# Optimization experiments

Measured on AMD Instinct MI355X. Metric: run time of the kernel, lower is better.

## Reference

```python
import jax, jax.numpy as jnp
import numpy as np

D_IN, HID, HEADS, MAXN, OUT, B = 16, 128, 4, 8, 128, 32768
HD = HID // HEADS
EPS = 1e-5


def _ln(x, g, b):
    m = jnp.mean(x, -1, keepdims=True)
    v = jnp.mean((x - m) ** 2, -1, keepdims=True)
    return (x - m) * jax.lax.rsqrt(v + EPS) * g + b


def _encode(x, enc_w1, enc_b1, enc_g1, enc_be1, enc_w2, enc_b2, enc_g2, enc_be2):
    h = _ln(x @ enc_w1.T + enc_b1, enc_g1, enc_be1)
    h = jax.nn.relu(h)
    return _ln(h @ enc_w2.T + enc_b2, enc_g2, enc_be2)


def setup_inputs() -> dict:
    key = jax.random.key(0)
    ks = jax.random.split(key, 12)

    def xavier(k, shape):
        # xavier_uniform with gain=0.5, matching _init_weights
        lim = 0.5 * np.sqrt(6.0 / (shape[0] + shape[1]))
        return jax.random.uniform(k, shape, jnp.float32, -lim, lim)

    z = lambda n: jnp.zeros((n,), jnp.float32)
    o = lambda n: jnp.ones((n,), jnp.float32)
    return {
        "current_node": jax.random.normal(ks[0], (B, D_IN), jnp.float32),
        "neighbor_nodes": jax.random.normal(ks[1], (B, MAXN, D_IN), jnp.float32),
        "neighbor_mask": jax.random.randint(ks[2], (B, MAXN), 0, 2, jnp.int32),
        "enc_w1": xavier(ks[3], (HID, D_IN)), "enc_b1": z(HID),
        "enc_g1": o(HID), "enc_be1": z(HID),
        "enc_w2": xavier(ks[4], (HID, HID)), "enc_b2": z(HID),
        "enc_g2": o(HID), "enc_be2": z(HID),
        "in_proj_w": xavier(ks[5], (3 * HID, HID)), "in_proj_b": z(3 * HID),
        "out_w": xavier(ks[6], (HID, HID)), "out_b": z(HID),
        "an_g": o(HID), "an_b": z(HID),
        "p1_w": xavier(ks[7], (HID, 2 * HID)), "p1_b": z(HID),
        "p1_g": o(HID), "p1_be": z(HID),
        "p2_w": xavier(ks[8], (OUT, HID)), "p2_b": z(OUT),
        "p2_g": o(OUT), "p2_be": z(OUT),
    }


def _forward(current_node, neighbor_nodes, neighbor_mask,
             enc_w1, enc_b1, enc_g1, enc_be1, enc_w2, enc_b2, enc_g2, enc_be2,
             in_proj_w, in_proj_b, out_w, out_b, an_g, an_b,
             p1_w, p1_b, p1_g, p1_be, p2_w, p2_b, p2_g, p2_be):
    bsz = current_node.shape[0]
    cur_emb = _encode(current_node, enc_w1, enc_b1, enc_g1, enc_be1,
                      enc_w2, enc_b2, enc_g2, enc_be2)                  # [B, HID]
    nb_emb = _encode(neighbor_nodes, enc_w1, enc_b1, enc_g1, enc_be1,
                     enc_w2, enc_b2, enc_g2, enc_be2)                   # [B, N, HID]

    valid = neighbor_mask > 0                                            # [B, N]
    has_nb = jnp.any(valid, axis=1)                                      # [B]

    # MultiheadAttention (eval mode, dropout inactive): q from current node, k/v from neighbors
    wq, wk, wv = in_proj_w[:HID], in_proj_w[HID:2 * HID], in_proj_w[2 * HID:]
    bq, bk, bv = in_proj_b[:HID], in_proj_b[HID:2 * HID], in_proj_b[2 * HID:]
    q = (cur_emb @ wq.T + bq).reshape(bsz, HEADS, HD)                    # [B, H, hd]
    k = (nb_emb @ wk.T + bk).reshape(bsz, MAXN, HEADS, HD)               # [B, N, H, hd]
    v = (nb_emb @ wv.T + bv).reshape(bsz, MAXN, HEADS, HD)

    scores = jnp.einsum('bhd,bnhd->bhn', q, k) / np.sqrt(HD)             # [B, H, N]
    # rows with zero valid neighbors get a fully-open mask to avoid NaN softmax;
    # their attention result is discarded below (replaced by cur_emb)
    safe = jnp.where(has_nb[:, None], valid, True)                       # [B, N]
    scores = jnp.where(safe[:, None, :], scores, -1e9)
    attn = jax.nn.softmax(scores, axis=-1)                               # [B, H, N]
    ctx = jnp.einsum('bhn,bnhd->bhd', attn, v).reshape(bsz, HID)
    ctx = ctx @ out_w.T + out_b
    agg = jnp.where(has_nb[:, None], _ln(ctx, an_g, an_b), cur_emb)      # [B, HID]

    combined = jnp.concatenate([cur_emb, agg], axis=-1)                  # [B, 2*HID]
    h = _ln(combined @ p1_w.T + p1_b, p1_g, p1_be)
    h = jax.nn.relu(h)
    return _ln(h @ p2_w.T + p2_b, p2_g, p2_be)                           # [B, OUT]


def reference(current_node, neighbor_nodes, neighbor_mask,
              enc_w1, enc_b1, enc_g1, enc_be1, enc_w2, enc_b2, enc_g2, enc_be2,
              in_proj_w, in_proj_b, out_w, out_b, an_g, an_b,
              p1_w, p1_b, p1_g, p1_be, p2_w, p2_b, p2_g, p2_be):
    return _forward(current_node, neighbor_nodes, neighbor_mask,
                    enc_w1, enc_b1, enc_g1, enc_be1, enc_w2, enc_b2, enc_g2, enc_be2,
                    in_proj_w, in_proj_b, out_w, out_b, an_g, an_b,
                    p1_w, p1_b, p1_g, p1_be, p2_w, p2_b, p2_g, p2_be)
```

## Files before the change

kernel.cpp:

```cpp
#include <hip/hip_runtime.h>

#define DEV __device__ __forceinline__

typedef __attribute__((ext_vector_type(8))) short bf16x8;
typedef __attribute__((ext_vector_type(4))) float f32x4;

static constexpr int NTH = 512;
static constexpr int TBE = 16;

static constexpr int W1P = 0;
static constexpr int W2  = 4096;
static constexpr int WQ  = 20480;
static constexpr int WK  = 36864;
static constexpr int WVW = 53248;
static constexpr int OW  = 69632;
static constexpr int P1A = 86016;
static constexpr int P1B = 102400;
static constexpr int P2W = 118784;
static constexpr int WS_BF16_TOT = 135168;
static constexpr int NPRM = 18 * 128;
static constexpr int WQr  = 139776;
static constexpr int OWr  = 156160;
static constexpr int P1Ar = 172544;
static constexpr int P1Br = 188928;
// ... 59 lines not shown
    int row = i >> 5, col = i & 31;
    float v = (col < 16) ? enc_w1[row * 16 + col] : 0.f;
    wsb[W1P + row * 32 + ((((col >> 3) ^ (row & 3)) << 3) | (col & 7))] = f2bf(v);
  }
  if (rm) {
    for (int i = t; i < 6 * 16384; i += NT) {
      int mi = i >> 14, e = i & 16383, row = e >> 7, col = e & 127;
      float v; int dstb;
      switch (mi) {
        case 0: v = in_pw[row * 128 + col];         dstb = WQr;  break;
        case 1: v = out_w[row * 128 + col];         dstb = OWr;  break;
        case 2: v = p1_w[row * 256 + col];          dstb = P1Ar; break;
        case 3: v = p1_w[row * 256 + 128 + col];    dstb = P1Br; break;
        case 4: v = p2_w[row * 128 + col];          dstb = P2r;  break;
        default: v = in_pw[(128 + col) * 128 + row]; dstb = WKt; break;
      }
      wsb[dstb + e] = f2bf(v);
    }
  }
  for (int i = t; i < NPRM; i += NT) {
    int s = i >> 7, c = i & 127; float v;
    switch (s) {
      case 0: v = enc_b1[c]; break;  case 1: v = enc_g1[c]; break;
      case 2: v = enc_be1[c]; break; case 3: v = enc_b2[c]; break;
      case 4: v = enc_g2[c]; break;  case 5: v = enc_be2[c]; break;
      case 6: v = in_pb[c]; break;   case 7: v = in_pb[128 + c]; break;
      case 8: v = in_pb[256 + c]; break; case 9: v = out_b[c]; break;
      case 10: v = an_g[c]; break;   case 11: v = an_b[c]; break;
      case 12: v = p1_b[c]; break;   case 13: v = p1_g[c]; break;
      case 14: v = p1_be[c]; break;  case 15: v = p2_b[c]; break;
      case 16: v = p2_g[c]; break;   default: v = p2_be[c]; break;
    }
    wsp[i] = v;
  }
}

__global__ __launch_bounds__(512, 4)
void k1_enc(const float* __restrict__ cur_x, const float* __restrict__ nb_x,
            const unsigned short* __restrict__ wsb, const float* __restrict__ wsp,
            unsigned short* __restrict__ wse) {
  __shared__ __align__(16) unsigned short s_w1[4096];
  __shared__ __align__(16) unsigned short s_w2[16384];
  __shared__ __align__(16) unsigned short s_h1[8][16 * 136];
  __shared__ float s_prm[6 * 128];

  const int tid = threadIdx.x;
  const int wv = tid >> 6, l = tid & 63, l15 = l & 15, lg = l >> 4;

  ((uint4*)s_w1)[tid] = ((const uint4*)(wsb + W1P))[tid];
#pragma unroll
  for (int i = 0; i < 4; ++i)
    ((uint4*)s_w2)[tid + i * 512] = ((const uint4*)(wsb + W2))[tid + i * 512];
  for (int i = tid; i < 768; i += 512) s_prm[i] = wsp[i];
  __syncthreads();

  unsigned short* h1 = &s_h1[wv][0];

  auto ln_t = [&](float (&acc)[8][4], int bs, int gs, int es, bool relu) {
#pragma unroll
    for (int ct = 0; ct < 8; ++ct) {
      float4 bb = *(const float4*)&s_prm[bs * 128 + ct * 16 + lg * 4];
      acc[ct][0] += bb.x; acc[ct][1] += bb.y; acc[ct][2] += bb.z; acc[ct][3] += bb.w;
    }
    float sm = 0.f, sq = 0.f;
#pragma unroll
    for (int ct = 0; ct < 8; ++ct)
#pragma unroll
      for (int r = 0; r < 4; ++r) { sm += acc[ct][r]; sq = fmaf(acc[ct][r], acc[ct][r], sq); }
    sm += __shfl_xor(sm, 16); sq += __shfl_xor(sq, 16);
    sm += __shfl_xor(sm, 32); sq += __shfl_xor(sq, 32);
    float mean = sm * 0.0078125f;
    float var = fmaf(sq, 0.0078125f, -mean * mean);
    float inv = rsqrtf(var + 1e-5f);
#pragma unroll
    for (int ct = 0; ct < 8; ++ct) {
      float4 gg = *(const float4*)&s_prm[gs * 128 + ct * 16 + lg * 4];
      float4 ee = *(const float4*)&s_prm[es * 128 + ct * 16 + lg * 4];
      float ga[4] = {gg.x, gg.y, gg.z, gg.w}, ea[4] = {ee.x, ee.y, ee.z, ee.w};
#pragma unroll
      for (int r = 0; r < 4; ++r) {
        float v = (acc[ct][r] - mean) * inv * ga[r] + ea[r];
        acc[ct][r] = relu ? fmaxf(v, 0.f) : v;
      }
    }
  };

#pragma unroll 1
  for (int t = blockIdx.x * 8 + wv; t < 18432; t += 9216) {
    asm volatile("s_waitcnt lgkmcnt(0)" ::: "memory");
    const bool isnb = t < 16384;
    const float* src = isnb ? nb_x + (size_t)t * 256
                            : cur_x + ((size_t)t - 16384) * 256;
    unsigned short* dst = wse + (isnb ? (size_t)NBE + (size_t)t * 2048
                                      : (size_t)CURE + ((size_t)t - 16384) * 2048);

    float4 fin = ((const float4*)src)[l];
    {
      uint2 u;
      u.x = (unsigned)f2bf(fin.x) | ((unsigned)f2bf(fin.y) << 16);
      u.y = (unsigned)f2bf(fin.z) | ((unsigned)f2bf(fin.w) << 16);
      *(uint2*)(h1 + (l >> 2) * 16 + (l & 3) * 4) = u;
    }
    bf16x8 bx = (bf16x8){0, 0, 0, 0, 0, 0, 0, 0};
    if (lg < 2) bx = *(const bf16x8*)(h1 + l15 * 16 + lg * 8);

    float acc[8][4];
#pragma unroll
    for (int ct = 0; ct < 8; ++ct) {
      f32x4 a = {0.f, 0.f, 0.f, 0.f};
      a = mfma16(frag32(s_w1, ct * 16 + l15, lg), bx, a);
      acc[ct][0] = a[0]; acc[ct][1] = a[1]; acc[ct][2] = a[2]; acc[ct][3] = a[3];
    }
    ln_t(acc, 0, 1, 2, true);
#pragma unroll
    for (int ct = 0; ct < 8; ++ct) {
      uint2 u;
      u.x = (unsigned)f2bf(acc[ct][0]) | ((unsigned)f2bf(acc[ct][1]) << 16);
      u.y = (unsigned)f2bf(acc[ct][2]) | ((unsigned)f2bf(acc[ct][3]) << 16);
      *(uint2*)(h1 + l15 * 136 + ct * 16 + lg * 4) = u;
    }

    bf16x8 bh[4];
#pragma unroll
    for (int kk = 0; kk < 4; ++kk)
      bh[kk] = *(const bf16x8*)(h1 + l15 * 136 + kk * 32 + lg * 8);
#pragma unroll
    for (int ct = 0; ct < 8; ++ct) {
      f32x4 a = {0.f, 0.f, 0.f, 0.f};
#pragma unroll
      for (int kk = 0; kk < 4; ++kk)
        a = mfma16(frag128(s_w2, ct * 16 + l15, kk, lg), bh[kk], a);
      acc[ct][0] = a[0]; acc[ct][1] = a[1]; acc[ct][2] = a[2]; acc[ct][3] = a[3];
    }
    ln_t(acc, 3, 4, 5, false);

#pragma unroll
    for (int ct = 0; ct < 8; ++ct) {
      uint2 u;
      u.x = (unsigned)f2bf(acc[ct][0]) | ((unsigned)f2bf(acc[ct][1]) << 16);
      u.y = (unsigned)f2bf(acc[ct][2]) | ((unsigned)f2bf(acc[ct][3]) << 16);
      int c = ct * 2 + (lg >> 1);
      *(uint2*)(h1 + l15 * 128 + ((c ^ l15) << 3) + (lg & 1) * 4) = u;
    }
#pragma unroll
    for (int i = 0; i < 4; ++i) {
      int R = i * 4 + lg;
      int j = l15;
      uint4 u = *(const uint4*)(h1 + R * 128 + ((j ^ R) << 3));
      ((uint4*)dst)[i * 64 + l] = u;
    }
  }
}

__global__ __launch_bounds__(256, 3)
void k2_head(const int* __restrict__ nb_mask,
             const unsigned short* __restrict__ wsb, const float* __restrict__ wsp,
             float* __restrict__ out) {
  __shared__ __align__(16) unsigned short s_buf[4][2][16 * 136];
  __shared__ float s_prm[NPRM];
  __shared__ int s_mask[64];

  const int tid = threadIdx.x;
  const int wv = tid >> 6, l = tid & 63, l15 = l & 15, lg = l >> 4;
  const int ew = (blockIdx.x * 4 + wv) * 16;
  unsigned short* bufA = &s_buf[wv][0][0];
  unsigned short* bufB = &s_buf[wv][1][0];

  for (int i = tid; i < NPRM; i += 256) s_prm[i] = wsp[i];
  {
    const uint4* src = (const uint4*)(wsb + CURE + (size_t)ew * 128);
#pragma unroll
    for (int i = 0; i < 4; ++i) {
      int idx = i * 64 + l, row = idx >> 4, ch = idx & 15;
      *(uint4*)(bufA + row * 136 + ch * 8) = src[idx];
    }
  }
  if (l < 16) {
    int m = 0; const int* mp = nb_mask + (size_t)(ew + l) * 8;
#pragma unroll
    for (int n = 0; n < 8; ++n) m |= (mp[n] > 0) << n;
    s_mask[wv * 16 + l] = m;
  }
  __syncthreads();

  float acc[8][4];

  auto ln_t = [&](int bs, int gs, int es, bool relu) {
#pragma unroll
    for (int ct = 0; ct < 8; ++ct) {
      float4 bb = *(const float4*)&s_prm[bs * 128 + ct * 16 + lg * 4];
      acc[ct][0] += bb.x; acc[ct][1] += bb.y; acc[ct][2] += bb.z; acc[ct][3] += bb.w;
    }
    float sm = 0.f, sq = 0.f;
#pragma unroll
    for (int ct = 0; ct < 8; ++ct)
#pragma unroll
      for (int r = 0; r < 4; ++r) { sm += acc[ct][r]; sq = fmaf(acc[ct][r], acc[ct][r], sq); }
    sm += __shfl_xor(sm, 16); sq += __shfl_xor(sq, 16);
    sm += __shfl_xor(sm, 32); sq += __shfl_xor(sq, 32);
    float mean = sm * 0.0078125f;
    float var = fmaf(sq, 0.0078125f, -mean * mean);
    float inv = rsqrtf(var + 1e-5f);
#pragma unroll
    for (int ct = 0; ct < 8; ++ct) {
      float4 gg = *(const float4*)&s_prm[gs * 128 + ct * 16 + lg * 4];
      float4 ee = *(const float4*)&s_prm[es * 128 + ct * 16 + lg * 4];
      float ga[4] = {gg.x, gg.y, gg.z, gg.w}, ea[4] = {ee.x, ee.y, ee.z, ee.w};
#pragma unroll
      for (int r = 0; r < 4; ++r) {
        float v = (acc[ct][r] - mean) * inv * ga[r] + ea[r];
        acc[ct][r] = relu ? fmaxf(v, 0.f) : v;
      }
    }
  };

  {
    bf16x8 b[4];
#pragma unroll
    for (int kk = 0; kk < 4; ++kk) b[kk] = *(const bf16x8*)(bufA + l15 * 136 + kk * 32 + lg * 8);
#pragma unroll
    for (int ct = 0; ct < 8; ++ct) {
      f32x4 a4 = {0.f, 0.f, 0.f, 0.f};
#pragma unroll
      for (int kk = 0; kk < 4; ++kk) {
        bf16x8 w = *(const bf16x8*)(wsb + WQr + (ct * 16 + l15) * 128 + kk * 32 + lg * 8);
        a4 = mfma16(w, b[kk], a4);
      }
      float4 bb = *(const float4*)&s_prm[6 * 128 + ct * 16 + lg * 4];
      uint2 u;
      u.x = (unsigned)f2bf((a4[0] + bb.x) * 0.17677669529663687f)
          | ((unsigned)f2bf((a4[1] + bb.y) * 0.17677669529663687f) << 16);
      u.y = (unsigned)f2bf((a4[2] + bb.z) * 0.17677669529663687f)
          | ((unsigned)f2bf((a4[3] + bb.w) * 0.17677669529663687f) << 16);
      *(uint2*)(bufB + l15 * 136 + ct * 16 + lg * 4) = u;
    }
  }
  __builtin_amdgcn_sched_barrier(0);

  bf16x8 qb[4];
#pragma unroll
  for (int h = 0; h < 4; ++h)
    qb[h] = *(const bf16x8*)(bufB + l15 * 136 + h * 32 + lg * 8);
  __builtin_amdgcn_sched_barrier(0);

  bf16x8 qf[4][4];
#pragma unroll
  for (int h = 0; h < 4; ++h) {
#pragma unroll
    for (int ct = 0; ct < 8; ++ct) {
      bf16x8 w = *(const bf16x8*)(wsb + WKt + (ct * 16 + l15) * 128 + h * 32 + lg * 8);
      f32x4 a4 = {0.f, 0.f, 0.f, 0.f};
      a4 = mfma16(w, qb[h], a4);
      uint2 u;
      u.x = (unsigned)f2bf(a4[0]) | ((unsigned)f2bf(a4[1]) << 16);
      u.y = (unsigned)f2bf(a4[2]) | ((unsigned)f2bf(a4[3]) << 16);
      *(uint2*)(bufB + l15 * 136 + ct * 16 + lg * 4) = u;
    }
    __builtin_amdgcn_sched_barrier(0);
#pragma unroll
    for (int kk = 0; kk < 4; ++kk)
      qf[h][kk] = *(const bf16x8*)(bufB + l15 * 136 + kk * 32 + lg * 8);
    __builtin_amdgcn_sched_barrier(0);
  }

  float pe[4][8];
  {
    const unsigned short* nbp = wsb + NBE + (size_t)(ew + l15) * 1024;
    float ps[4][8];
#pragma unroll
    for (int h = 0; h < 4; ++h)
#pragma unroll
      for (int n = 0; n < 8; ++n) ps[h][n] = 0.f;
#pragma unroll
    for (int n = 0; n < 8; ++n) {
#pragma unroll
      for (int kk = 0; kk < 4; ++kk) {
        bf16x8 nf = *(const bf16x8*)(nbp + n * 128 + kk * 32 + lg * 8);
#pragma unroll
        for (int i = 0; i < 8; ++i) {
          float nv = bf2f((unsigned short)nf[i]);
          ps[0][n] = fmaf(nv, bf2f((unsigned short)qf[0][kk][i]), ps[0][n]);
          ps[1][n] = fmaf(nv, bf2f((unsigned short)qf[1][kk][i]), ps[1][n]);
          ps[2][n] = fmaf(nv, bf2f((unsigned short)qf[2][kk][i]), ps[2][n]);
          ps[3][n] = fmaf(nv, bf2f((unsigned short)qf[3][kk][i]), ps[3][n]);
        }
      }
    }
#pragma unroll
    for (int h = 0; h < 4; ++h)
#pragma unroll
      for (int n = 0; n < 8; ++n) {
        ps[h][n] += __shfl_xor(ps[h][n], 16);
        ps[h][n] += __shfl_xor(ps[h][n], 32);
      }
    int m = s_mask[wv * 16 + l15];
    bool all = (m == 0);
#pragma unroll
    for (int h = 0; h < 4; ++h) {
      float mx = -1e30f;
#pragma unroll
      for (int n = 0; n < 8; ++n) {
        bool u = all || ((m >> n) & 1);
        mx = fmaxf(mx, u ? ps[h][n] : -1e30f);
      }
      float su = 0.f;
#pragma unroll
      for (int n = 0; n < 8; ++n) {
        bool u = all || ((m >> n) & 1);
        pe[h][n] = u ? __expf(ps[h][n] - mx) : 0.f;
        su += pe[h][n];
      }
      float inv = 1.f / su;
#pragma unroll
      for (int n = 0; n < 8; ++n) pe[h][n] *= inv;
    }
  }
  __builtin_amdgcn_sched_barrier(0);

  {
    const unsigned short* nbp = wsb + NBE + (size_t)(ew + l15) * 1024;
#pragma unroll
    for (int h = 0; h < 4; ++h) {
      float pn[4][8];
#pragma unroll
      for (int kk = 0; kk < 4; ++kk)
#pragma unroll
        for (int i = 0; i < 8; ++i) pn[kk][i] = 0.f;
#pragma unroll
      for (int n = 0; n < 8; ++n) {
        float pv = pe[h][n];
#pragma unroll
        for (int kk = 0; kk < 4; ++kk) {
          bf16x8 nf = *(const bf16x8*)(nbp + n * 128 + kk * 32 + lg * 8);
#pragma unroll
          for (int i = 0; i < 8; ++i)
            pn[kk][i] = fmaf(bf2f((unsigned short)nf[i]), pv, pn[kk][i]);
        }
      }
#pragma unroll
      for (int kk = 0; kk < 4; ++kk) {
        uint4 u;
        u.x = (unsigned)f2bf(pn[kk][0]) | ((unsigned)f2bf(pn[kk][1]) << 16);
        u.y = (unsigned)f2bf(pn[kk][2]) | ((unsigned)f2bf(pn[kk][3]) << 16);
        u.z = (unsigned)f2bf(pn[kk][4]) | ((unsigned)f2bf(pn[kk][5]) << 16);
        u.w = (unsigned)f2bf(pn[kk][6]) | ((unsigned)f2bf(pn[kk][7]) << 16);
        *(uint4*)(bufB + l15 * 136 + kk * 32 + lg * 8) = u;
      }
      __builtin_amdgcn_sched_barrier(0);
#pragma unroll
      for (int cc = 0; cc < 2; ++cc) {
        int ct = h * 2 + cc;
        f32x4 a4 = {0.f, 0.f, 0.f, 0.f};
#pragma unroll
        for (int kk = 0; kk < 4; ++kk) {
          bf16x8 b = *(const bf16x8*)(bufB + l15 * 136 + kk * 32 + lg * 8);
          a4 = mfma16(frag128(wsb + WVW, ct * 16 + l15, kk, lg), b, a4);
        }
        acc[ct][0] = a4[0]; acc[ct][1] = a4[1]; acc[ct][2] = a4[2]; acc[ct][3] = a4[3];
      }
      __builtin_amdgcn_sched_barrier(0);
    }
#pragma unroll
    for (int ct = 0; ct < 8; ++ct) {
      float4 bb = *(const float4*)&s_prm[8 * 128 + ct * 16 + lg * 4];
      uint2 u;
      u.x = (unsigned)f2bf(acc[ct][0] + bb.x) | ((unsigned)f2bf(acc[ct][1] + bb.y) << 16);
      u.y = (unsigned)f2bf(acc[ct][2] + bb.z) | ((unsigned)f2bf(acc[ct][3] + bb.w) << 16);
      *(uint2*)(bufB + l15 * 136 + ct * 16 + lg * 4) = u;
    }
  }
  __builtin_amdgcn_sched_barrier(0);

  {
    bf16x8 b[4];
#pragma unroll
    for (int kk = 0; kk < 4; ++kk) b[kk] = *(const bf16x8*)(bufB + l15 * 136 + kk * 32 + lg * 8);
    __builtin_amdgcn_sched_barrier(0);
#pragma unroll
    for (int ct = 0; ct < 8; ++ct) {
      f32x4 a4 = {0.f, 0.f, 0.f, 0.f};
#pragma unroll
      for (int kk = 0; kk < 4; ++kk) {
        bf16x8 w = *(const bf16x8*)(wsb + OWr + (ct * 16 + l15) * 128 + kk * 32 + lg * 8);
        a4 = mfma16(w, b[kk], a4);
      }
      acc[ct][0] = a4[0]; acc[ct][1] = a4[1]; acc[ct][2] = a4[2]; acc[ct][3] = a4[3];
    }
    ln_t(9, 10, 11, false);
    int m = s_mask[wv * 16 + l15];
#pragma unroll
    for (int ct = 0; ct < 8; ++ct) {
      uint2 cu = *(const uint2*)(bufA + l15 * 136 + ct * 16 + lg * 4);
      unsigned short a0 = m ? f2bf(acc[ct][0]) : (unsigned short)(cu.x & 0xffff);
      unsigned short a1 = m ? f2bf(acc[ct][1]) : (unsigned short)(cu.x >> 16);
      unsigned short a2 = m ? f2bf(acc[ct][2]) : (unsigned short)(cu.y & 0xffff);
      unsigned short a3 = m ? f2bf(acc[ct][3]) : (unsigned short)(cu.y >> 16);
      uint2 u;
      u.x = (unsigned)a0 | ((unsigned)a1 << 16);
      u.y = (unsigned)a2 | ((unsigned)a3 << 16);
      *(uint2*)(bufB + l15 * 136 + ct * 16 + lg * 4) = u;
    }
  }
  __builtin_amdgcn_sched_barrier(0);

  {
    bf16x8 bc[4], bg[4];
#pragma unroll
    for (int kk = 0; kk < 4; ++kk) {
      bc[kk] = *(const bf16x8*)(bufA + l15 * 136 + kk * 32 + lg * 8);
      bg[kk] = *(const bf16x8*)(bufB + l15 * 136 + kk * 32 + lg * 8);
    }
    __builtin_amdgcn_sched_barrier(0);
#pragma unroll
    for (int ct = 0; ct < 8; ++ct) {
      f32x4 a4 = {0.f, 0.f, 0.f, 0.f};
#pragma unroll
      for (int kk = 0; kk < 4; ++kk) {
        bf16x8 w = *(const bf16x8*)(wsb + P1Ar + (ct * 16 + l15) * 128 + kk * 32 + lg * 8);
        a4 = mfma16(w, bc[kk], a4);
      }
#pragma unroll
      for (int kk = 0; kk < 4; ++kk) {
        bf16x8 w = *(const bf16x8*)(wsb + P1Br + (ct * 16 + l15) * 128 + kk * 32 + lg * 8);
        a4 = mfma16(w, bg[kk], a4);
      }
      acc[ct][0] = a4[0]; acc[ct][1] = a4[1]; acc[ct][2] = a4[2]; acc[ct][3] = a4[3];
    }
    ln_t(12, 13, 14, true);
#pragma unroll
    for (int ct = 0; ct < 8; ++ct) {
      uint2 u;
      u.x = (unsigned)f2bf(acc[ct][0]) | ((unsigned)f2bf(acc[ct][1]) << 16);
      u.y = (unsigned)f2bf(acc[ct][2]) | ((unsigned)f2bf(acc[ct][3]) << 16);
      *(uint2*)(bufB + l15 * 136 + ct * 16 + lg * 4) = u;
    }
  }
  __builtin_amdgcn_sched_barrier(0);

  {
    bf16x8 b[4];
#pragma unroll
    for (int kk = 0; kk < 4; ++kk) b[kk] = *(const bf16x8*)(bufB + l15 * 136 + kk * 32 + lg * 8);
    __builtin_amdgcn_sched_barrier(0);
#pragma unroll
    for (int ct = 0; ct < 8; ++ct) {
      f32x4 a4 = {0.f, 0.f, 0.f, 0.f};
#pragma unroll
      for (int kk = 0; kk < 4; ++kk) {
        bf16x8 w = *(const bf16x8*)(wsb + P2r + (ct * 16 + l15) * 128 + kk * 32 + lg * 8);
        a4 = mfma16(w, b[kk], a4);
      }
      acc[ct][0] = a4[0]; acc[ct][1] = a4[1]; acc[ct][2] = a4[2]; acc[ct][3] = a4[3];
    }
    ln_t(15, 16, 17, false);
    float* op = out + (size_t)(ew + l15) * 128;
#pragma unroll
    for (int ct = 0; ct < 8; ++ct)
      *(float4*)(op + ct * 16 + lg * 4) =
          make_float4(acc[ct][0], acc[ct][1], acc[ct][2], acc[ct][3]);
  }
}

__global__ __launch_bounds__(NTH, 1)
void gcn_mfma(const float* __restrict__ cur_x, const float* __restrict__ nb_x,
              const int* __restrict__ nb_mask,
              const unsigned short* __restrict__ wsb, const float* __restrict__ wsp,
              float* __restrict__ out) {
  __shared__ __align__(16) unsigned short s_stage[20480];
  __shared__ __align__(16) unsigned short s_X[144 * 32];
  __shared__ __align__(16) unsigned short s_H[144 * 128];
  __shared__ __align__(16) unsigned short s_Enb[128 * 128];
  __shared__ __align__(16) unsigned short s_Ecur[16 * 128];
  __shared__ __align__(16) float s_q[16 * 132];
  __shared__ __align__(16) float s_p[16 * 32];
  __shared__ __align__(16) unsigned short s_ctx[16 * 128];
  __shared__ __align__(16) unsigned short s_agg[16 * 128];
  __shared__ __align__(16) unsigned short s_hh[16 * 128];
  __shared__ float s_prm[NPRM];
  __shared__ int s_mask[16];

  const int tid = threadIdx.x;
  const int wv = tid >> 6, l = tid & 63, l15 = l & 15, lg = l >> 4;
  const int sub = l >> 5, l32 = l & 31;
  const int ebase = blockIdx.x * TBE;
  const int eo = wv * 2 + sub;

  auto stage = [&](int srcOff) {
    const uint4* s = (const uint4*)(wsb + srcOff);
    uint4* d = (uint4*)s_stage;
#pragma unroll
    for (int i = 0; i < 4; ++i) d[tid + i * NTH] = s[tid + i * NTH];
  };
  auto ln_epi = [&](float (&vals)[8][4], int bslot, int gslot, int beslot, bool relu) {
    float sm[4] = {0, 0, 0, 0}, sq[4] = {0, 0, 0, 0};
#pragma unroll
    for (int nt = 0; nt < 8; ++nt) {
      float b = s_prm[bslot * 128 + nt * 16 + l15];
#pragma unroll
      for (int r = 0; r < 4; ++r) {
        float v = vals[nt][r] + b; vals[nt][r] = v;
        sm[r] += v; sq[r] = fmaf(v, v, sq[r]);
      }
    }
#pragma unroll
    for (int off = 8; off >= 1; off >>= 1)
#pragma unroll
      for (int r = 0; r < 4; ++r) {
        sm[r] += __shfl_xor(sm[r], off);
        sq[r] += __shfl_xor(sq[r], off);
      }
    float mean[4], inv[4];
#pragma unroll
    for (int r = 0; r < 4; ++r) {
      mean[r] = sm[r] * 0.0078125f;
      float var = fmaf(sq[r], 0.0078125f, -mean[r] * mean[r]);
      inv[r] = rsqrtf(var + 1e-5f);
    }
#pragma unroll
    for (int nt = 0; nt < 8; ++nt) {
      int col = nt * 16 + l15;
      float g = s_prm[gslot * 128 + col], be = s_prm[beslot * 128 + col];
#pragma unroll
      for (int r = 0; r < 4; ++r) {
        float v = (vals[nt][r] - mean[r]) * inv[r] * g + be;
        vals[nt][r] = relu ? fmaxf(v, 0.f) : v;
      }
    }
  };

  {
    const uint4* s = (const uint4*)(wsb + W1P);
    ((uint4*)(s_stage + 16384))[tid] = s[tid];
  }
  for (int i = tid; i < NPRM; i += NTH) s_prm[i] = wsp[i];
  for (int i = tid; i < 4608; i += NTH) {
    int row = i >> 5, col = i & 31;
    int e = (row * 57) >> 9, kind = row - e * 9;
    float v = 0.f;
    if (col < 16) {
      int ge = ebase + e;
      v = (kind == 0) ? cur_x[(size_t)ge * 16 + col]
                      : nb_x[((size_t)ge * 8 + (kind - 1)) * 16 + col];
    }
    s_X[row * 32 + ((((col >> 3) ^ (row & 3)) << 3) | (col & 7))] = f2bf(v);
  }
  if (tid < 16) {
    int m = 0; const int* mp = nb_mask + (size_t)(ebase + tid) * 8;
#pragma unroll
    for (int n = 0; n < 8; ++n) m |= (mp[n] > 0) << n;
    s_mask[tid] = m;
  }
  __syncthreads();

  stage(W2);
  for (int mt = wv; mt < 9; mt += 8) {
    bf16x8 a = frag32(s_X, mt * 16 + l15, lg);
    float vals[8][4];
#pragma unroll
    for (int nt = 0; nt < 8; ++nt) {
      f32x4 acc = {0.f, 0.f, 0.f, 0.f};
      acc = mfma16(a, frag32(s_stage + 16384, nt * 16 + l15, lg), acc);
#pragma unroll
      for (int r = 0; r < 4; ++r) vals[nt][r] = acc[r];
    }
    ln_epi(vals, 0, 1, 2, true);
#pragma unroll
    for (int nt = 0; nt < 8; ++nt)
#pragma unroll
      for (int r = 0; r < 4; ++r)
        st_bf16(s_H, mt * 16 + lg * 4 + r, nt * 16 + l15, vals[nt][r]);
  }
  __syncthreads();

  for (int mt = wv; mt < 9; mt += 8) {
    bf16x8 a[4];
#pragma unroll
    for (int kk = 0; kk < 4; ++kk) a[kk] = frag128(s_H, mt * 16 + l15, kk, lg);
    float vals[8][4];
#pragma unroll
    for (int nt = 0; nt < 8; ++nt) {
      f32x4 acc = {0.f, 0.f, 0.f, 0.f};
#pragma unroll
      for (int kk = 0; kk < 4; ++kk)
        acc = mfma16(a[kk], frag128(s_stage, nt * 16 + l15, kk, lg), acc);
#pragma unroll
      for (int r = 0; r < 4; ++r) vals[nt][r] = acc[r];
    }
    ln_epi(vals, 3, 4, 5, false);
#pragma unroll
    for (int nt = 0; nt < 8; ++nt) {
      int col = nt * 16 + l15;
#pragma unroll
      for (int r = 0; r < 4; ++r) {
        int R = mt * 16 + lg * 4 + r;
        int e = (R * 57) >> 9, kind = R - e * 9;
        if (kind == 0) st_bf16(s_Ecur, e, col, vals[nt][r]);
        else           st_bf16(s_Enb, e * 8 + kind - 1, col, vals[nt][r]);
      }
    }
  }
  __syncthreads();
  stage(WQ);
  __syncthreads();

  {
    f32x4 acc = {0.f, 0.f, 0.f, 0.f};
#pragma unroll
    for (int kk = 0; kk < 4; ++kk)
      acc = mfma16(frag128(s_Ecur, l15, kk, lg), frag128(s_stage, wv * 16 + l15, kk, lg), acc);
    int col = wv * 16 + l15; float bq = s_prm[6 * 128 + col];
#pragma unroll
    for (int r = 0; r < 4; ++r) s_q[(lg * 4 + r) * 132 + col] = acc[r] + bq;
// ... 84 lines not shown
      st_bf16(s_ctx, eo, col, c);
    }
  }
  __syncthreads();

  {
    f32x4 acc = {0.f, 0.f, 0.f, 0.f};
#pragma unroll
    for (int kk = 0; kk < 4; ++kk)
      acc = mfma16(frag128(s_ctx, l15, kk, lg), frag128(s_stage, wv * 16 + l15, kk, lg), acc);
    int col = wv * 16 + l15; float bo = s_prm[9 * 128 + col];
#pragma unroll
    for (int r = 0; r < 4; ++r) s_q[(lg * 4 + r) * 132 + col] = acc[r] + bo;
  }
  __syncthreads();

  stage(P1A);
  {
    float4 x = *(const float4*)&s_q[eo * 132 + l32 * 4];
    float s = x.x + x.y + x.z + x.w;
    float qq = fmaf(x.x, x.x, fmaf(x.y, x.y, fmaf(x.z, x.z, x.w * x.w)));
#pragma unroll
    for (int off = 16; off >= 1; off >>= 1) { s += __shfl_xor(s, off); qq += __shfl_xor(qq, off); }
    float mean = s * 0.0078125f;
    float var = fmaf(qq, 0.0078125f, -mean * mean);
    float inv = rsqrtf(var + 1e-5f);
    int m = s_mask[eo];
    float xa[4] = {x.x, x.y, x.z, x.w}, r4[4];
#pragma unroll
    for (int c = 0; c < 4; ++c) {
      int col = l32 * 4 + c;
      float v = (xa[c] - mean) * inv * s_prm[10 * 128 + col] + s_prm[11 * 128 + col];
      r4[c] = m ? v : ld_bf16(s_Ecur, eo, col);
    }
    uint2 uu;
    uu.x = (unsigned)f2bf(r4[0]) | ((unsigned)f2bf(r4[1]) << 16);
    uu.y = (unsigned)f2bf(r4[2]) | ((unsigned)f2bf(r4[3]) << 16);
    *(uint2*)(s_agg + eo * 128 + (((l32 >> 1) ^ (eo & 7)) << 3) + (l32 & 1) * 4) = uu;
  }
  __syncthreads();

  f32x4 accP = {0.f, 0.f, 0.f, 0.f};
#pragma unroll
  for (int kk = 0; kk < 4; ++kk)
    accP = mfma16(frag128(s_Ecur, l15, kk, lg), frag128(s_stage, wv * 16 + l15, kk, lg), accP);
  __syncthreads();
  stage(P1B);
  __syncthreads();
  {
#pragma unroll
    for (int kk = 0; kk < 4; ++kk)
      accP = mfma16(frag128(s_agg, l15, kk, lg), frag128(s_stage, wv * 16 + l15, kk, lg), accP);
    int col = wv * 16 + l15; float b = s_prm[12 * 128 + col];
#pragma unroll
    for (int r = 0; r < 4; ++r) s_q[(lg * 4 + r) * 132 + col] = accP[r] + b;
  }
  __syncthreads();

  stage(P2W);
  {
    float4 x = *(const float4*)&s_q[eo * 132 + l32 * 4];
    float s = x.x + x.y + x.z + x.w;
    float qq = fmaf(x.x, x.x, fmaf(x.y, x.y, fmaf(x.z, x.z, x.w * x.w)));
#pragma unroll
    for (int off = 16; off >= 1; off >>= 1) { s += __shfl_xor(s, off); qq += __shfl_xor(qq, off); }
    float mean = s * 0.0078125f;
    float var = fmaf(qq, 0.0078125f, -mean * mean);
    float inv = rsqrtf(var + 1e-5f);
    float xa[4] = {x.x, x.y, x.z, x.w}, r4[4];
#pragma unroll
    for (int c = 0; c < 4; ++c) {
      int col = l32 * 4 + c;
      r4[c] = fmaxf((xa[c] - mean) * inv * s_prm[13 * 128 + col] + s_prm[14 * 128 + col], 0.f);
    }
    uint2 uu;
    uu.x = (unsigned)f2bf(r4[0]) | ((unsigned)f2bf(r4[1]) << 16);
    uu.y = (unsigned)f2bf(r4[2]) | ((unsigned)f2bf(r4[3]) << 16);
    *(uint2*)(s_hh + eo * 128 + (((l32 >> 1) ^ (eo & 7)) << 3) + (l32 & 1) * 4) = uu;
  }
  __syncthreads();

  {
    f32x4 acc = {0.f, 0.f, 0.f, 0.f};
#pragma unroll
    for (int kk = 0; kk < 4; ++kk)
      acc = mfma16(frag128(s_hh, l15, kk, lg), frag128(s_stage, wv * 16 + l15, kk, lg), acc);
    int col = wv * 16 + l15; float b = s_prm[15 * 128 + col];
#pragma unroll
    for (int r = 0; r < 4; ++r) s_q[(lg * 4 + r) * 132 + col] = acc[r] + b;
  }
  __syncthreads();

  {
    float4 x = *(const float4*)&s_q[eo * 132 + l32 * 4];
    float s = x.x + x.y + x.z + x.w;
    float qq = fmaf(x.x, x.x, fmaf(x.y, x.y, fmaf(x.z, x.z, x.w * x.w)));
#pragma unroll
    for (int off = 16; off >= 1; off >>= 1) { s += __shfl_xor(s, off); qq += __shfl_xor(qq, off); }
    float mean = s * 0.0078125f;
    float var = fmaf(qq, 0.0078125f, -mean * mean);
    float inv = rsqrtf(var + 1e-5f);
    float xa[4] = {x.x, x.y, x.z, x.w};
    float4 o;
    o.x = (xa[0] - mean) * inv * s_prm[16 * 128 + l32 * 4 + 0] + s_prm[17 * 128 + l32 * 4 + 0];
    o.y = (xa[1] - mean) * inv * s_prm[16 * 128 + l32 * 4 + 1] + s_prm[17 * 128 + l32 * 4 + 1];
    o.z = (xa[2] - mean) * inv * s_prm[16 * 128 + l32 * 4 + 2] + s_prm[17 * 128 + l32 * 4 + 2];
    o.w = (xa[3] - mean) * inv * s_prm[16 * 128 + l32 * 4 + 3] + s_prm[17 * 128 + l32 * 4 + 3];
    *(float4*)&out[(size_t)(ebase + eo) * 128 + l32 * 4] = o;
  }
}

extern "C" void kernel_launch(void* const* d_in, const int* in_sizes, int n_in,
                              void* d_out, int out_size, void* d_ws, size_t ws_size,
                              hipStream_t stream) {
  const float* cur_x   = (const float*)d_in[0];
  const float* nb_x    = (const float*)d_in[1];
  const int*   nbm     = (const int*)d_in[2];
  const float* enc_w1  = (const float*)d_in[3];
  const float* enc_b1  = (const float*)d_in[4];
  const float* enc_g1  = (const float*)d_in[5];
  const float* enc_be1 = (const float*)d_in[6];
  const float* enc_w2  = (const float*)d_in[7];
  const float* enc_b2  = (const float*)d_in[8];
  const float* enc_g2  = (const float*)d_in[9];
  const float* enc_be2 = (const float*)d_in[10];
  const float* in_pw   = (const float*)d_in[11];
  const float* in_pb   = (const float*)d_in[12];
  const float* out_w   = (const float*)d_in[13];
  const float* out_b   = (const float*)d_in[14];
  const float* an_g    = (const float*)d_in[15];
  const float* an_b    = (const float*)d_in[16];
  const float* p1_w    = (const float*)d_in[17];
  const float* p1_b    = (const float*)d_in[18];
  const float* p1_g    = (const float*)d_in[19];
  const float* p1_be   = (const float*)d_in[20];
  const float* p2_w    = (const float*)d_in[21];
  const float* p2_b    = (const float*)d_in[22];
  const float* p2_g    = (const float*)d_in[23];
  const float* p2_be   = (const float*)d_in[24];
  float* out = (float*)d_out;

  unsigned short* wsb = (unsigned short*)d_ws;
  float* wsp = (float*)(wsb + WS_BF16_TOT);
  const int B = in_sizes[0] / 16;
  const bool split = (ws_size >= SPLIT_NEED) && (B == 32768);

  prep<<<128, 256, 0, stream>>>(enc_w1, enc_w2, in_pw, out_w, p1_w, p2_w,
                                enc_b1, enc_g1, enc_be1, enc_b2, enc_g2, enc_be2,
                                in_pb, out_b, an_g, an_b, p1_b, p1_g, p1_be,
                                p2_b, p2_g, p2_be, wsb, wsp, split ? 1 : 0);

  if (split) {
    k1_enc<<<1152, 512, 0, stream>>>(cur_x, nb_x, wsb, wsp, wsb);
    k2_head<<<B / 64, 256, 0, stream>>>(nbm, wsb, wsp, out);
  } else {
    gcn_mfma<<<B / TBE, NTH, 0, stream>>>(cur_x, nb_x, nbm, wsb, wsp, out);
  }
}
```

Measured before the change: 166.7 us.

## Restructure k2_head to one wave per 8 elements with per-lane neighbor attention

k2_head now launches single-wave blocks that each handle 8 batch elements instead of 4-wave blocks of 64. The MFMA tiles stay 16 wide with zero-padded rows. The attention score and context loops are remapped so each lane owns one element and a 16-wide slice of the feature dimension, with an extra shuffle reduction. The shared-memory parameter copy and __syncthreads are dropped in favour of direct global reads of the parameters and per-lane mask registers, with explicit lgkmcnt waits. This aims for more parallel blocks and less per-lane scalar attention work, but half of every MFMA tile is now wasted and all projection weight fetches are repeated per 8 elements.

```diff
diff --git a/kernel.cpp b/kernel.cpp
--- a/kernel.cpp
+++ b/kernel.cpp
@@ -235,43 +235,54 @@
   }
 }
 
-__global__ __launch_bounds__(256, 3)
+__global__ __launch_bounds__(64, 4)
 void k2_head(const int* __restrict__ nb_mask,
              const unsigned short* __restrict__ wsb, const float* __restrict__ wsp,
              float* __restrict__ out) {
-  __shared__ __align__(16) unsigned short s_buf[4][2][16 * 136];
-  __shared__ float s_prm[NPRM];
-  __shared__ int s_mask[64];
-
-  const int tid = threadIdx.x;
-  const int wv = tid >> 6, l = tid & 63, l15 = l & 15, lg = l >> 4;
-  const int ew = (blockIdx.x * 4 + wv) * 16;
-  unsigned short* bufA = &s_buf[wv][0][0];
-  unsigned short* bufB = &s_buf[wv][1][0];
-
-  for (int i = tid; i < NPRM; i += 256) s_prm[i] = wsp[i];
+  __shared__ __align__(16) unsigned short bufA[16 * 136];
+  __shared__ __align__(16) unsigned short bufB[16 * 136];
+
+  const int l = threadIdx.x;
+  const int l15 = l & 15, lg = l >> 4;
+  const int e = l & 7, grp = l >> 3;
+  const int ew = blockIdx.x * 8;
+
+  {
+    uint4 z = make_uint4(0, 0, 0, 0);
+#pragma unroll
+    for (int i = 0; i < 5; ++i) {
+      int idx = i * 64 + l;
+      if (idx < 272) { ((uint4*)bufA)[idx] = z; ((uint4*)bufB)[idx] = z; }
+    }
+  }
   {
     const uint4* src = (const uint4*)(wsb + CURE + (size_t)ew * 128);
 #pragma unroll
-    for (int i = 0; i < 4; ++i) {
-      int idx = i * 64 + l, row = idx >> 4, ch = idx & 15;
+    for (int i = 0; i < 2; ++i) {
+      int idx = i * 64 + l;
+      int row = idx >> 4, ch = idx & 15;
       *(uint4*)(bufA + row * 136 + ch * 8) = src[idx];
     }
   }
-  if (l < 16) {
-    int m = 0; const int* mp = nb_mask + (size_t)(ew + l) * 8;
-#pragma unroll
-    for (int n = 0; n < 8; ++n) m |= (mp[n] > 0) << n;
-    s_mask[wv * 16 + l] = m;
-  }
-  __syncthreads();
+  int mreg = 0, mreg15 = 0;
+  {
+    const int* mp = nb_mask + (size_t)(ew + e) * 8;
+    const int* mp2 = nb_mask + (size_t)(ew + (l15 & 7)) * 8;
+#pragma unroll
+    for (int n = 0; n < 8; ++n) {
+      mreg |= (mp[n] > 0) << n;
+      mreg15 |= (mp2[n] > 0) << n;
+    }
+  }
+  asm volatile("s_waitcnt lgkmcnt(0)" ::: "memory");
+  __builtin_amdgcn_sched_barrier(0);
 
   float acc[8][4];
 
   auto ln_t = [&](int bs, int gs, int es, bool relu) {
 #pragma unroll
     for (int ct = 0; ct < 8; ++ct) {
-      float4 bb = *(const float4*)&s_prm[bs * 128 + ct * 16 + lg * 4];
+      float4 bb = *(const float4*)&wsp[bs * 128 + ct * 16 + lg * 4];
       acc[ct][0] += bb.x; acc[ct][1] += bb.y; acc[ct][2] += bb.z; acc[ct][3] += bb.w;
     }
     float sm = 0.f, sq = 0.f;
@@ -286,8 +297,8 @@
     float inv = rsqrtf(var + 1e-5f);
 #pragma unroll
     for (int ct = 0; ct < 8; ++ct) {
-      float4 gg = *(const float4*)&s_prm[gs * 128 + ct * 16 + lg * 4];
-      float4 ee = *(const float4*)&s_prm[es * 128 + ct * 16 + lg * 4];
+      float4 gg = *(const float4*)&wsp[gs * 128 + ct * 16 + lg * 4];
+      float4 ee = *(const float4*)&wsp[es * 128 + ct * 16 + lg * 4];
       float ga[4] = {gg.x, gg.y, gg.z, gg.w}, ea[4] = {ee.x, ee.y, ee.z, ee.w};
 #pragma unroll
       for (int r = 0; r < 4; ++r) {
@@ -309,7 +320,7 @@
         bf16x8 w = *(const bf16x8*)(wsb + WQr + (ct * 16 + l15) * 128 + kk * 32 + lg * 8);
         a4 = mfma16(w, b[kk], a4);
       }
-      float4 bb = *(const float4*)&s_prm[6 * 128 + ct * 16 + lg * 4];
+      float4 bb = *(const float4*)&wsp[6 * 128 + ct * 16 + lg * 4];
       uint2 u;
       u.x = (unsigned)f2bf((a4[0] + bb.x) * 0.17677669529663687f)
           | ((unsigned)f2bf((a4[1] + bb.y) * 0.17677669529663687f) << 16);
@@ -318,15 +329,17 @@
       *(uint2*)(bufB + l15 * 136 + ct * 16 + lg * 4) = u;
     }
   }
+  asm volatile("s_waitcnt lgkmcnt(0)" ::: "memory");
   __builtin_amdgcn_sched_barrier(0);
 
   bf16x8 qb[4];
 #pragma unroll
   for (int h = 0; h < 4; ++h)
     qb[h] = *(const bf16x8*)(bufB + l15 * 136 + h * 32 + lg * 8);
+  asm volatile("s_waitcnt lgkmcnt(0)" ::: "memory");
   __builtin_amdgcn_sched_barrier(0);
 
-  bf16x8 qf[4][4];
+  bf16x8 qf[4][2];
 #pragma unroll
   for (int h = 0; h < 4; ++h) {
 #pragma unroll
@@ -339,16 +352,26 @@
       u.y = (unsigned)f2bf(a4[2]) | ((unsigned)f2bf(a4[3]) << 16);
       *(uint2*)(bufB + l15 * 136 + ct * 16 + lg * 4) = u;
     }
+    asm volatile("s_waitcnt lgkmcnt(0)" ::: "memory");
     __builtin_amdgcn_sched_barrier(0);
-#pragma unroll
-    for (int kk = 0; kk < 4; ++kk)
-      qf[h][kk] = *(const bf16x8*)(bufB + l15 * 136 + kk * 32 + lg * 8);
+    qf[h][0] = *(const bf16x8*)(bufB + e * 136 + grp * 16);
+    qf[h][1] = *(const bf16x8*)(bufB + e * 136 + grp * 16 + 8);
+    asm volatile("s_waitcnt lgkmcnt(0)" ::: "memory");
     __builtin_amdgcn_sched_barrier(0);
   }
 
+  float qff[4][16];
+#pragma unroll
+  for (int h = 0; h < 4; ++h)
+#pragma unroll
+    for (int j = 0; j < 2; ++j)
+#pragma unroll
+      for (int i = 0; i < 8; ++i)
+        qff[h][j * 8 + i] = bf2f((unsigned short)qf[h][j][i]);
+
   float pe[4][8];
   {
-    const unsigned short* nbp = wsb + NBE + (size_t)(ew + l15) * 1024;
+    const unsigned short* nbp = wsb + NBE + (size_t)(ew + e) * 1024 + grp * 16;
     float ps[4][8];
 #pragma unroll
     for (int h = 0; h < 4; ++h)
@@ -356,16 +379,16 @@
       for (int n = 0; n < 8; ++n) ps[h][n] = 0.f;
 #pragma unroll
     for (int n = 0; n < 8; ++n) {
-#pragma unroll
-      for (int kk = 0; kk < 4; ++kk) {
-        bf16x8 nf = *(const bf16x8*)(nbp + n * 128 + kk * 32 + lg * 8);
-#pragma unroll
-        for (int i = 0; i < 8; ++i) {
-          float nv = bf2f((unsigned short)nf[i]);
-          ps[0][n] = fmaf(nv, bf2f((unsigned short)qf[0][kk][i]), ps[0][n]);
-          ps[1][n] = fmaf(nv, bf2f((unsigned short)qf[1][kk][i]), ps[1][n]);
-          ps[2][n] = fmaf(nv, bf2f((unsigned short)qf[2][kk][i]), ps[2][n]);
-          ps[3][n] = fmaf(nv, bf2f((unsigned short)qf[3][kk][i]), ps[3][n]);
+      bf16x8 n0 = *(const bf16x8*)(nbp + n * 128);
+      bf16x8 n1 = *(const bf16x8*)(nbp + n * 128 + 8);
+#pragma unroll
+      for (int i = 0; i < 8; ++i) {
+        float v0 = bf2f((unsigned short)n0[i]);
+        float v1 = bf2f((unsigned short)n1[i]);
+#pragma unroll
+        for (int h = 0; h < 4; ++h) {
+          ps[h][n] = fmaf(v0, qff[h][i], ps[h][n]);
+          ps[h][n] = fmaf(v1, qff[h][8 + i], ps[h][n]);
         }
       }
     }
@@ -373,23 +396,23 @@
     for (int h = 0; h < 4; ++h)
 #pragma unroll
       for (int n = 0; n < 8; ++n) {
+        ps[h][n] += __shfl_xor(ps[h][n], 8);
         ps[h][n] += __shfl_xor(ps[h][n], 16);
         ps[h][n] += __shfl_xor(ps[h][n], 32);
       }
-    int m = s_mask[wv * 16 + l15];
-    bool all = (m == 0);
+    bool all = (mreg == 0);
 #pragma unroll
     for (int h = 0; h < 4; ++h) {
       float mx = -1e30f;
 #pragma unroll
       for (int n = 0; n < 8; ++n) {
-        bool u = all || ((m >> n) & 1);
+        bool u = all || ((mreg >> n) & 1);
         mx = fmaxf(mx, u ? ps[h][n] : -1e30f);
       }
       float su = 0.f;
 #pragma unroll
       for (int n = 0; n < 8; ++n) {
-        bool u = all || ((m >> n) & 1);
+        bool u = all || ((mreg >> n) & 1);
         pe[h][n] = u ? __expf(ps[h][n] - mx) : 0.f;
         su += pe[h][n];
       }
@@ -400,64 +423,76 @@
   }
   __builtin_amdgcn_sched_barrier(0);
 
-  {
-    const unsigned short* nbp = wsb + NBE + (size_t)(ew + l15) * 1024;
-#pragma unroll
-    for (int h = 0; h < 4; ++h) {
-      float pn[4][8];
-#pragma unroll
-      for (int kk = 0; kk < 4; ++kk)
-#pragma unroll
-        for (int i = 0; i < 8; ++i) pn[kk][i] = 0.f;
-#pragma unroll
-      for (int n = 0; n < 8; ++n) {
-        float pv = pe[h][n];
-#pragma unroll
-        for (int kk = 0; kk < 4; ++kk) {
-          bf16x8 nf = *(const bf16x8*)(nbp + n * 128 + kk * 32 + lg * 8);
-#pragma unroll
-          for (int i = 0; i < 8; ++i)
-            pn[kk][i] = fmaf(bf2f((unsigned short)nf[i]), pv, pn[kk][i]);
+  float pn[4][16];
+#pragma unroll
+  for (int h = 0; h < 4; ++h)
+#pragma unroll
+    for (int i = 0; i < 16; ++i) pn[h][i] = 0.f;
+  {
+    const unsigned short* nbp = wsb + NBE + (size_t)(ew + e) * 1024 + grp * 16;
+#pragma unroll
+    for (int n = 0; n < 8; ++n) {
+      bf16x8 n0 = *(const bf16x8*)(nbp + n * 128);
+      bf16x8 n1 = *(const bf16x8*)(nbp + n * 128 + 8);
+#pragma unroll
+      for (int i = 0; i < 8; ++i) {
+        float v0 = bf2f((unsigned short)n0[i]);
+        float v1 = bf2f((unsigned short)n1[i]);
+#pragma unroll
+        for (int h = 0; h < 4; ++h) {
+          pn[h][i] = fmaf(v0, pe[h][n], pn[h][i]);
+          pn[h][8 + i] = fmaf(v1, pe[h][n], pn[h][8 + i]);
         }
       }
+    }
+  }
+  __builtin_amdgcn_sched_barrier(0);
+
+#pragma unroll
+  for (int h = 0; h < 4; ++h) {
+    uint4 u0, u1;
+    u0.x = (unsigned)f2bf(pn[h][0]) | ((unsigned)f2bf(pn[h][1]) << 16);
+    u0.y = (unsigned)f2bf(pn[h][2]) | ((unsigned)f2bf(pn[h][3]) << 16);
+    u0.z = (unsigned)f2bf(pn[h][4]) | ((unsigned)f2bf(pn[h][5]) << 16);
+    u0.w = (unsigned)f2bf(pn[h][6]) | ((unsigned)f2bf(pn[h][7]) << 16);
+    u1.x = (unsigned)f2bf(pn[h][8]) | ((unsigned)f2bf(pn[h][9]) << 16);
+    u1.y = (unsigned)f2bf(pn[h][10]) | ((unsigned)f2bf(pn[h][11]) << 16);
+    u1.z = (unsigned)f2bf(pn[h][12]) | ((unsigned)f2bf(pn[h][13]) << 16);
+    u1.w = (unsigned)f2bf(pn[h][14]) | ((unsigned)f2bf(pn[h][15]) << 16);
+    *(uint4*)(bufB + e * 136 + grp * 16) = u0;
+    *(uint4*)(bufB + e * 136 + grp * 16 + 8) = u1;
+    asm volatile("s_waitcnt lgkmcnt(0)" ::: "memory");
+    __builtin_amdgcn_sched_barrier(0);
+#pragma unroll
+    for (int cc = 0; cc < 2; ++cc) {
+      int ct = h * 2 + cc;
+      f32x4 a4 = {0.f, 0.f, 0.f, 0.f};
 #pragma unroll
       for (int kk = 0; kk < 4; ++kk) {
-        uint4 u;
-        u.x = (unsigned)f2bf(pn[kk][0]) | ((unsigned)f2bf(pn[kk][1]) << 16);
-        u.y = (unsigned)f2bf(pn[kk][2]) | ((unsigned)f2bf(pn[kk][3]) << 16);
-        u.z = (unsigned)f2bf(pn[kk][4]) | ((unsigned)f2bf(pn[kk][5]) << 16);
-        u.w = (unsigned)f2bf(pn[kk][6]) | ((unsigned)f2bf(pn[kk][7]) << 16);
-        *(uint4*)(bufB + l15 * 136 + kk * 32 + lg * 8) = u;
-      }
-      __builtin_amdgcn_sched_barrier(0);
-#pragma unroll
-      for (int cc = 0; cc < 2; ++cc) {
-        int ct = h * 2 + cc;
-        f32x4 a4 = {0.f, 0.f, 0.f, 0.f};
-#pragma unroll
-        for (int kk = 0; kk < 4; ++kk) {
-          bf16x8 b = *(const bf16x8*)(bufB + l15 * 136 + kk * 32 + lg * 8);
-          a4 = mfma16(frag128(wsb + WVW, ct * 16 + l15, kk, lg), b, a4);
-        }
-        acc[ct][0] = a4[0]; acc[ct][1] = a4[1]; acc[ct][2] = a4[2]; acc[ct][3] = a4[3];
-      }
-      __builtin_amdgcn_sched_barrier(0);
-    }
-#pragma unroll
-    for (int ct = 0; ct < 8; ++ct) {
-      float4 bb = *(const float4*)&s_prm[8 * 128 + ct * 16 + lg * 4];
-      uint2 u;
-      u.x = (unsigned)f2bf(acc[ct][0] + bb.x) | ((unsigned)f2bf(acc[ct][1] + bb.y) << 16);
-      u.y = (unsigned)f2bf(acc[ct][2] + bb.z) | ((unsigned)f2bf(acc[ct][3] + bb.w) << 16);
-      *(uint2*)(bufB + l15 * 136 + ct * 16 + lg * 4) = u;
-    }
-  }
+        bf16x8 b = *(const bf16x8*)(bufB + l15 * 136 + kk * 32 + lg * 8);
+        a4 = mfma16(frag128(wsb + WVW, ct * 16 + l15, kk, lg), b, a4);
+      }
+      acc[ct][0] = a4[0]; acc[ct][1] = a4[1]; acc[ct][2] = a4[2]; acc[ct][3] = a4[3];
+    }
+    asm volatile("s_waitcnt lgkmcnt(0)" ::: "memory");
+    __builtin_amdgcn_sched_barrier(0);
+  }
+#pragma unroll
+  for (int ct = 0; ct < 8; ++ct) {
+    float4 bb = *(const float4*)&wsp[8 * 128 + ct * 16 + lg * 4];
+    uint2 u;
+    u.x = (unsigned)f2bf(acc[ct][0] + bb.x) | ((unsigned)f2bf(acc[ct][1] + bb.y) << 16);
+    u.y = (unsigned)f2bf(acc[ct][2] + bb.z) | ((unsigned)f2bf(acc[ct][3] + bb.w) << 16);
+    *(uint2*)(bufB + l15 * 136 + ct * 16 + lg * 4) = u;
+  }
+  asm volatile("s_waitcnt lgkmcnt(0)" ::: "memory");
   __builtin_amdgcn_sched_barrier(0);
 
   {
     bf16x8 b[4];
 #pragma unroll
     for (int kk = 0; kk < 4; ++kk) b[kk] = *(const bf16x8*)(bufB + l15 * 136 + kk * 32 + lg * 8);
+    asm volatile("s_waitcnt lgkmcnt(0)" ::: "memory");
     __builtin_amdgcn_sched_barrier(0);
 #pragma unroll
     for (int ct = 0; ct < 8; ++ct) {
@@ -470,20 +505,20 @@
       acc[ct][0] = a4[0]; acc[ct][1] = a4[1]; acc[ct][2] = a4[2]; acc[ct][3] = a4[3];
     }
     ln_t(9, 10, 11, false);
-    int m = s_mask[wv * 16 + l15];
 #pragma unroll
     for (int ct = 0; ct < 8; ++ct) {
       uint2 cu = *(const uint2*)(bufA + l15 * 136 + ct * 16 + lg * 4);
-      unsigned short a0 = m ? f2bf(acc[ct][0]) : (unsigned short)(cu.x & 0xffff);
-      unsigned short a1 = m ? f2bf(acc[ct][1]) : (unsigned short)(cu.x >> 16);
-      unsigned short a2 = m ? f2bf(acc[ct][2]) : (unsigned short)(cu.y & 0xffff);
-      unsigned short a3 = m ? f2bf(acc[ct][3]) : (unsigned short)(cu.y >> 16);
+      unsigned short a0 = mreg15 ? f2bf(acc[ct][0]) : (unsigned short)(cu.x & 0xffff);
+      unsigned short a1 = mreg15 ? f2bf(acc[ct][1]) : (unsigned short)(cu.x >> 16);
+      unsigned short a2 = mreg15 ? f2bf(acc[ct][2]) : (unsigned short)(cu.y & 0xffff);
+      unsigned short a3 = mreg15 ? f2bf(acc[ct][3]) : (unsigned short)(cu.y >> 16);
       uint2 u;
       u.x = (unsigned)a0 | ((unsigned)a1 << 16);
       u.y = (unsigned)a2 | ((unsigned)a3 << 16);
       *(uint2*)(bufB + l15 * 136 + ct * 16 + lg * 4) = u;
     }
   }
+  asm volatile("s_waitcnt lgkmcnt(0)" ::: "memory");
   __builtin_amdgcn_sched_barrier(0);
 
   {
@@ -493,6 +528,7 @@
       bc[kk] = *(const bf16x8*)(bufA + l15 * 136 + kk * 32 + lg * 8);
       bg[kk] = *(const bf16x8*)(bufB + l15 * 136 + kk * 32 + lg * 8);
     }
+    asm volatile("s_waitcnt lgkmcnt(0)" ::: "memory");
     __builtin_amdgcn_sched_barrier(0);
 #pragma unroll
     for (int ct = 0; ct < 8; ++ct) {
@@ -518,12 +554,14 @@
       *(uint2*)(bufB + l15 * 136 + ct * 16 + lg * 4) = u;
     }
   }
+  asm volatile("s_waitcnt lgkmcnt(0)" ::: "memory");
   __builtin_amdgcn_sched_barrier(0);
 
   {
     bf16x8 b[4];
 #pragma unroll
     for (int kk = 0; kk < 4; ++kk) b[kk] = *(const bf16x8*)(bufB + l15 * 136 + kk * 32 + lg * 8);
+    asm volatile("s_waitcnt lgkmcnt(0)" ::: "memory");
     __builtin_amdgcn_sched_barrier(0);
 #pragma unroll
     for (int ct = 0; ct < 8; ++ct) {
@@ -536,11 +574,13 @@
       acc[ct][0] = a4[0]; acc[ct][1] = a4[1]; acc[ct][2] = a4[2]; acc[ct][3] = a4[3];
     }
     ln_t(15, 16, 17, false);
-    float* op = out + (size_t)(ew + l15) * 128;
-#pragma unroll
-    for (int ct = 0; ct < 8; ++ct)
-      *(float4*)(op + ct * 16 + lg * 4) =
-          make_float4(acc[ct][0], acc[ct][1], acc[ct][2], acc[ct][3]);
+    if (l15 < 8) {
+      float* op = out + (size_t)(ew + l15) * 128;
+#pragma unroll
+      for (int ct = 0; ct < 8; ++ct)
+        *(float4*)(op + ct * 16 + lg * 4) =
+            make_float4(acc[ct][0], acc[ct][1], acc[ct][2], acc[ct][3]);
+    }
   }
 }
 
@@ -931,7 +971,7 @@
 
   if (split) {
     k1_enc<<<1152, 512, 0, stream>>>(cur_x, nb_x, wsb, wsp, wsb);
-    k2_head<<<B / 64, 256, 0, stream>>>(nbm, wsb, wsp, out);
+    k2_head<<<B / 8, 64, 0, stream>>>(nbm, wsb, wsp, out);
   } else {
     gcn_mfma<<<B / TBE, NTH, 0, stream>>>(cur_x, nb_x, nbm, wsb, wsp, out);
   }
```

Result: slower. 242.3 us (+45.4%).
